# Optimization experiments

Measured on AMD Instinct MI355X. Metric: run time of the kernel, lower is better.

## Reference

```python
import jax, jax.numpy as jnp
import numpy as np

B, T, D, E, F = 4, 2048, 1024, 8, 1024

def setup_inputs() -> dict:
    key = jax.random.key(0)
    ks = jax.random.split(key, 5)
    s = lambda d: 1.0 / np.sqrt(d)
    return {
        "x": jax.random.normal(ks[0], (B, T, D), dtype=jnp.float32),
        "router_kernel_DE": jax.random.normal(ks[1], (D, E), dtype=jnp.float32) * s(D),
        "kernel_gating_EDF": jax.random.normal(ks[2], (E, D, F), dtype=jnp.float32) * s(D),
        "kernel_up_EDF": jax.random.normal(ks[3], (E, D, F), dtype=jnp.float32) * s(D),
        "kernel_down_EFD": jax.random.normal(ks[4], (E, F, D), dtype=jnp.float32) * s(F),
        "top_k": 2,
    }

def reference(x, router_kernel_DE, kernel_gating_EDF, kernel_up_EDF, kernel_down_EFD, top_k):
    # ---- Router ----
    router_logits_BTE = jnp.einsum('BTD,DE->BTE', x, router_kernel_DE)
    probs_BTE = jax.nn.softmax(router_logits_BTE.astype(jnp.float32), axis=-1)
    weights_BTX, selected_BTX = jax.lax.top_k(probs_BTE, top_k)
    # module re-normalizes top-k weights with a second softmax (faithful)
    norm_weights_BTX = jax.nn.softmax(weights_BTX, axis=-1)
    # ---- combine weights to dense per-expert weights ----
    one_hot_BTXE = jax.nn.one_hot(selected_BTX, num_classes=E, dtype=jnp.float32)
    full_weights_BTE = jnp.sum(one_hot_BTXE * norm_weights_BTX[..., None], axis=2)
    # ---- dense all-experts MLP (apply_expert_weight_before_computation=False) ----
    gating_BTEF = jnp.einsum('BTD,EDF->BTEF', x, kernel_gating_EDF)
    up_BTEF = jnp.einsum('BTD,EDF->BTEF', x, kernel_up_EDF)
    fuse_BTEF = jax.nn.silu(gating_BTEF) * up_BTEF
    down_BTED = jnp.einsum('BTEF,EFD->BTED', fuse_BTEF, kernel_down_EFD)
    out_BTD = jnp.einsum('BTED,BTE->BTD', down_BTED, full_weights_BTE)
    return out_BTD
```

## Files before the change

kernel.cpp:

```cpp
#include <hip/hip_runtime.h>
#include <hip/hip_bf16.h>
#include <math.h>

#define NTOK 8192
#define D_DIM 1024
#define E_DIM 8
#define F_DIM 1024

#define CNT_STRIDE 32

typedef __attribute__((ext_vector_type(8))) short bf16x8;
typedef __attribute__((ext_vector_type(4))) float f32x4;

typedef const __attribute__((address_space(1))) unsigned int* as1_uint_ptr;
typedef __attribute__((address_space(3))) unsigned int* as3_uint_ptr;

__device__ __forceinline__ void async_load16(const void* g, void* l) {
    __builtin_amdgcn_global_load_lds((as1_uint_ptr)g, (as3_uint_ptr)l, 16, 0, 0);
}

__device__ __forceinline__ float bf2f(unsigned short b) {
    unsigned int u = ((unsigned int)b) << 16;
    return __builtin_bit_cast(float, u);
}
__device__ __forceinline__ unsigned short f2bf(float f) {
    __hip_bfloat16 h = __float2bfloat16(f);
    return __builtin_bit_cast(unsigned short, h);
}


__global__ __launch_bounds__(512) void router_cast_kernel(
    const float* __restrict__ x,
    const float* __restrict__ Wr,
    int* __restrict__ cnt,
    int* __restrict__ tok_of,
    float* __restrict__ wt2,
    unsigned short* __restrict__ xb)
{
    __shared__ int lcnt[E_DIM];
    __shared__ int lbase[E_DIM];
    __shared__ int lbuf[E_DIM][64];

    const int tid = threadIdx.x;
    const int wv = tid >> 6;
    const int lane = tid & 63;
    if (tid < E_DIM) lcnt[tid] = 0;
    __syncthreads();

    #pragma unroll
    for (int it = 0; it < 4; ++it) {
        const int t = blockIdx.x * 32 + wv * 4 + it;
        const float* xrow = x + (size_t)t * D_DIM;
        unsigned short* xbrow = xb + (size_t)t * D_DIM;

        float p[E_DIM];
        #pragma unroll
        for (int e = 0; e < E_DIM; ++e) p[e] = 0.f;

        #pragma unroll
        for (int i = 0; i < 4; ++i) {
            const int d = i * 256 + lane * 4;
            float4 v = *(const float4*)(xrow + d);
            ushort4 o;
            o.x = f2bf(v.x); o.y = f2bf(v.y); o.z = f2bf(v.z); o.w = f2bf(v.w);
            *(ushort4*)(xbrow + d) = o;
            const float* wr = Wr + (size_t)d * E_DIM;
            float xv[4] = {v.x, v.y, v.z, v.w};
            #pragma unroll
            for (int q = 0; q < 4; ++q) {
                float4 w0 = *(const float4*)(wr + q * 8);
                float4 w1 = *(const float4*)(wr + q * 8 + 4);
                p[0] += xv[q] * w0.x; p[1] += xv[q] * w0.y;
                p[2] += xv[q] * w0.z; p[3] += xv[q] * w0.w;
                p[4] += xv[q] * w1.x; p[5] += xv[q] * w1.y;
                p[6] += xv[q] * w1.z; p[7] += xv[q] * w1.w;
            }
        }

        #pragma unroll
        for (int off = 32; off > 0; off >>= 1) {
            #pragma unroll
            for (int e = 0; e < E_DIM; ++e)
                p[e] += __shfl_xor(p[e], off, 64);
        }

        if (lane == 0) {
            float m = p[0];
            #pragma unroll
            for (int e = 1; e < E_DIM; ++e) m = fmaxf(m, p[e]);
            float pr[E_DIM], sum = 0.f;
            #pragma unroll
            for (int e = 0; e < E_DIM; ++e) { pr[e] = expf(p[e] - m); sum += pr[e]; }
            float inv = 1.f / sum;
            #pragma unroll
            for (int e = 0; e < E_DIM; ++e) pr[e] *= inv;
            int e0 = 0;
            #pragma unroll
            for (int e = 1; e < E_DIM; ++e) if (pr[e] > pr[e0]) e0 = e;
            int e1 = (e0 == 0) ? 1 : 0;
            #pragma unroll
            for (int e = 0; e < E_DIM; ++e) { if (e != e0 && pr[e] > pr[e1]) e1 = e; }
            float b = expf(pr[e1] - pr[e0]);
            float w0 = 1.f / (1.f + b);
            float w1 = b / (1.f + b);
            int p0 = atomicAdd(&lcnt[e0], 1);
            lbuf[e0][p0] = t * 2 + 0;
            int p1 = atomicAdd(&lcnt[e1], 1);
            lbuf[e1][p1] = t * 2 + 1;
            wt2[t * 2 + 0] = w0;
            wt2[t * 2 + 1] = w1;
        }
    }
    __syncthreads();
    if (tid < E_DIM) lbase[tid] = atomicAdd(&cnt[tid * CNT_STRIDE], lcnt[tid]);
    __syncthreads();
    #pragma unroll
    for (int e = 0; e < E_DIM; ++e) {
        int n = lcnt[e];
        if (tid < n) tok_of[e * NTOK + lbase[e] + tid] = lbuf[e][tid];
    }
}

__global__ __launch_bounds__(256) void transpose_cast_kernel(
    const float* __restrict__ Wg, const float* __restrict__ Wu,
    const float* __restrict__ Wd,
    unsigned short* __restrict__ WgT, unsigned short* __restrict__ WuT,
    unsigned short* __restrict__ WdT)
{
    const int m = blockIdx.z;
    const float* src;
    unsigned short* dst;
    if (m < 8)       { src = Wg + (size_t)m * 1048576;        dst = WgT + (size_t)m * 1048576; }
    else if (m < 16) { src = Wu + (size_t)(m - 8) * 1048576;  dst = WuT + (size_t)(m - 8) * 1048576; }
    else             { src = Wd + (size_t)(m - 16) * 1048576; dst = WdT + (size_t)(m - 16) * 1048576; }

    const int c0 = blockIdx.x * 64;
    const int r0 = blockIdx.y * 64;
    __shared__ float tile[64][65];
    const int tid = threadIdx.x;
    const int tr = tid >> 4;
    const int tc = (tid & 15) * 4;
    #pragma unroll
    for (int p = 0; p < 4; ++p) {
        float4 v = *(const float4*)(src + (size_t)(r0 + p * 16 + tr) * 1024 + c0 + tc);
        tile[p * 16 + tr][tc + 0] = v.x;
        tile[p * 16 + tr][tc + 1] = v.y;
        tile[p * 16 + tr][tc + 2] = v.z;
        tile[p * 16 + tr][tc + 3] = v.w;
    }
    __syncthreads();
    const int orow = tid >> 3;
    const int ocol = (tid & 7) * 8;
    #pragma unroll
    for (int p = 0; p < 2; ++p) {
        int fr = p * 32 + orow;
        union { unsigned short s[8]; uint4 v; } pk;
        #pragma unroll
        for (int q = 0; q < 8; ++q) pk.s[q] = f2bf(tile[ocol + q][fr]);
        *(uint4*)&dst[(size_t)(c0 + fr) * 1024 + r0 + ocol] = pk.v;
    }
}

__global__ __launch_bounds__(256, 2) void gateup_mfma(
    const unsigned short* __restrict__ xb,
    const unsigned short* __restrict__ WgT,
    const unsigned short* __restrict__ WuT,
    const int* __restrict__ cnt,
    const int* __restrict__ tok_of,
    unsigned short* __restrict__ H)
{
    const int e = blockIdx.y;
    const int rowTile = blockIdx.x >> 3;
    const int colTile = blockIdx.x & 7;
    const int rows = cnt[e * CNT_STRIDE];
    const int rowBase = rowTile * 128;
    if (rowBase >= rows) return;
    const int n0 = colTile * 128;

    __shared__ short As[128 * 32];
    __shared__ short Bg[128 * 32];
    __shared__ short Bu[128 * 32];
    __shared__ int toks[128];

    const int tid = threadIdx.x;
    if (tid < 128) {
        int idx = rowBase + tid;
        toks[tid] = tok_of[e * NTOK + (idx < rows ? idx : rows - 1)];
    }
    __syncthreads();

    const int lane = tid & 63;
    const int w = tid >> 6;
    const int seg0 = w * 2, seg1 = w * 2 + 1;
    const int sr = lane >> 2;
    const int swz = (sr >> 1) & 3;
    const int sk = ((lane & 3) ^ swz) * 8;

    const int ar0 = seg0 * 16 + sr;
    const int ar1 = seg1 * 16 + sr;
    const unsigned short* aG0 = xb + (size_t)(toks[ar0] >> 1) * D_DIM + sk;
    const unsigned short* aG1 = xb + (size_t)(toks[ar1] >> 1) * D_DIM + sk;
    const unsigned short* WgTe = WgT + (size_t)e * F_DIM * D_DIM;
    const unsigned short* WuTe = WuT + (size_t)e * F_DIM * D_DIM;
    const unsigned short* gG0 = WgTe + (size_t)(n0 + ar0) * D_DIM + sk;
    const unsigned short* gG1 = WgTe + (size_t)(n0 + ar1) * D_DIM + sk;
    const unsigned short* uG0 = WuTe + (size_t)(n0 + ar0) * D_DIM + sk;
    const unsigned short* uG1 = WuTe + (size_t)(n0 + ar1) * D_DIM + sk;

    short* aL0 = &As[seg0 * 512];
    short* aL1 = &As[seg1 * 512];
    short* gL0 = &Bg[seg0 * 512];
    short* gL1 = &Bg[seg1 * 512];
    short* uL0 = &Bu[seg0 * 512];
    short* uL1 = &Bu[seg1 * 512];

    const int mseg = (w >> 1) * 4;
    const int nseg = (w & 1) * 4;
    const int mbase = (w >> 1) * 64;
    const int nbase = (w & 1) * 64;
    const int fr = lane & 15;
    const int rd = (4 * fr + ((lane >> 4) ^ ((fr >> 1) & 3))) * 8;

    f32x4 accg[4][4], accu[4][4];
    #pragma unroll
    for (int i = 0; i < 4; ++i)
        #pragma unroll
        for (int j = 0; j < 4; ++j) { accg[i][j] = (f32x4)(0.f); accu[i][j] = (f32x4)(0.f); }

    for (int k0 = 0; k0 < D_DIM; k0 += 32) {
        async_load16(aG0 + k0, aL0);
        async_load16(aG1 + k0, aL1);
        async_load16(gG0 + k0, gL0);
        async_load16(gG1 + k0, gL1);
        async_load16(uG0 + k0, uL0);
        async_load16(uG1 + k0, uL1);
        __syncthreads();

        bf16x8 a[4], g[4], u[4];
        #pragma unroll
        for (int i = 0; i < 4; ++i)
            a[i] = *(const bf16x8*)&As[(mseg + i) * 512 + rd];
        #pragma unroll
        for (int j = 0; j < 4; ++j) {
            g[j] = *(const bf16x8*)&Bg[(nseg + j) * 512 + rd];
            u[j] = *(const bf16x8*)&Bu[(nseg + j) * 512 + rd];
        }
        #pragma unroll
        for (int i = 0; i < 4; ++i)
            #pragma unroll
            for (int j = 0; j < 4; ++j) {
                accg[i][j] = __builtin_amdgcn_mfma_f32_16x16x32_bf16(a[i], g[j], accg[i][j], 0, 0, 0);
                accu[i][j] = __builtin_amdgcn_mfma_f32_16x16x32_bf16(a[i], u[j], accu[i][j], 0, 0, 0);
            }
        __syncthreads();
    }

    const int erow = (lane >> 4) * 4;
    #pragma unroll
    for (int i = 0; i < 4; ++i) {
        #pragma unroll
        for (int r = 0; r < 4; ++r) {
            int row = mbase + i * 16 + erow + r;
            int idx = rowBase + row;
            if (idx < rows) {
                int tok2 = toks[row];
                unsigned short* hrow = H + (size_t)tok2 * F_DIM + n0 + nbase;
                #pragma unroll
                for (int j = 0; j < 4; ++j) {
                    float gg = accg[i][j][r];
                    float uu = accu[i][j][r];
                    float h = gg / (1.f + __expf(-gg)) * uu;
                    hrow[j * 16 + fr] = f2bf(h);
                }
            }
        }
    }
}

__global__ __launch_bounds__(256, 2) void down_mfma(
    const unsigned short* __restrict__ H,
    const unsigned short* __restrict__ WdT,
    const int* __restrict__ cnt,
    const int* __restrict__ tok_of,
    unsigned short* __restrict__ Hd)
{
    const int e = blockIdx.y;
    const int rowTile = blockIdx.x >> 3;
    const int colTile = blockIdx.x & 7;
    const int rows = cnt[e * CNT_STRIDE];
    const int rowBase = rowTile * 128;
    if (rowBase >= rows) return;
    const int n0 = colTile * 128;

    __shared__ short As[128 * 32];
    __shared__ short Bs[128 * 32];
    __shared__ int toks[128];

    const int tid = threadIdx.x;
    if (tid < 128) {
        int idx = rowBase + tid;
        toks[tid] = tok_of[e * NTOK + (idx < rows ? idx : rows - 1)];
    }
    __syncthreads();

    const int lane = tid & 63;
    const int w = tid >> 6;
    const int seg0 = w * 2, seg1 = w * 2 + 1;
    const int sr = lane >> 2;
    const int swz = (sr >> 1) & 3;
    const int sk = ((lane & 3) ^ swz) * 8;

    const int ar0 = seg0 * 16 + sr;
    const int ar1 = seg1 * 16 + sr;
    const unsigned short* aG0 = H + (size_t)toks[ar0] * F_DIM + sk;
    const unsigned short* aG1 = H + (size_t)toks[ar1] * F_DIM + sk;
    const unsigned short* WdTe = WdT + (size_t)e * D_DIM * F_DIM;
    const unsigned short* bG0 = WdTe + (size_t)(n0 + ar0) * F_DIM + sk;
    const unsigned short* bG1 = WdTe + (size_t)(n0 + ar1) * F_DIM + sk;

    short* aL0 = &As[seg0 * 512];
    short* aL1 = &As[seg1 * 512];
    short* bL0 = &Bs[seg0 * 512];
    short* bL1 = &Bs[seg1 * 512];

    const int mseg = (w >> 1) * 4;
    const int nseg = (w & 1) * 4;
    const int mbase = (w >> 1) * 64;
    const int nbase = (w & 1) * 64;
    const int fr = lane & 15;
    const int rd = (4 * fr + ((lane >> 4) ^ ((fr >> 1) & 3))) * 8;

    f32x4 acc[4][4];
    #pragma unroll
    for (int i = 0; i < 4; ++i)
        #pragma unroll
        for (int j = 0; j < 4; ++j) acc[i][j] = (f32x4)(0.f);

    for (int k0 = 0; k0 < F_DIM; k0 += 32) {
        async_load16(aG0 + k0, aL0);
        async_load16(aG1 + k0, aL1);
        async_load16(bG0 + k0, bL0);
        async_load16(bG1 + k0, bL1);
        __syncthreads();

        bf16x8 a[4], b[4];
        #pragma unroll
        for (int i = 0; i < 4; ++i)
            a[i] = *(const bf16x8*)&As[(mseg + i) * 512 + rd];
        #pragma unroll
        for (int j = 0; j < 4; ++j)
            b[j] = *(const bf16x8*)&Bs[(nseg + j) * 512 + rd];
        #pragma unroll
        for (int i = 0; i < 4; ++i)
            #pragma unroll
            for (int j = 0; j < 4; ++j)
                acc[i][j] = __builtin_amdgcn_mfma_f32_16x16x32_bf16(a[i], b[j], acc[i][j], 0, 0, 0);
        __syncthreads();
    }

    const int erow = (lane >> 4) * 4;
    #pragma unroll
    for (int i = 0; i < 4; ++i) {
        #pragma unroll
        for (int r = 0; r < 4; ++r) {
            int row = mbase + i * 16 + erow + r;
            int idx = rowBase + row;
            if (idx < rows) {
                int tok2 = toks[row];
                unsigned short* orow = Hd + (size_t)tok2 * D_DIM + n0 + nbase;
                #pragma unroll
                for (int j = 0; j < 4; ++j)
                    orow[j * 16 + fr] = f2bf(acc[i][j][r]);
            }
        }
    }
}

__global__ __launch_bounds__(256) void combine_kernel(
    const unsigned short* __restrict__ Hd,
    const float* __restrict__ wt2,
    float* __restrict__ out)
{
    const int t = blockIdx.x;
    const int tid = threadIdx.x;
    const float w0 = wt2[2 * t];
    const float w1 = wt2[2 * t + 1];
    const int c = tid * 4;
    ushort4 a = *(const ushort4*)&Hd[(size_t)(2 * t) * D_DIM + c];
    ushort4 b = *(const ushort4*)&Hd[(size_t)(2 * t + 1) * D_DIM + c];
    float4 o;
    o.x = w0 * bf2f(a.x) + w1 * bf2f(b.x);
    o.y = w0 * bf2f(a.y) + w1 * bf2f(b.y);
    o.z = w0 * bf2f(a.z) + w1 * bf2f(b.z);
    o.w = w0 * bf2f(a.w) + w1 * bf2f(b.w);
    *(float4*)(out + (size_t)t * D_DIM + c) = o;
}

extern "C" void kernel_launch(void* const* d_in, const int* in_sizes, int n_in,
                              void* d_out, int out_size, void* d_ws, size_t ws_size,
                              hipStream_t stream) {
    const float* x  = (const float*)d_in[0];
    const float* Wr = (const float*)d_in[1];
    const float* Wg = (const float*)d_in[2];
    const float* Wu = (const float*)d_in[3];
    const float* Wd = (const float*)d_in[4];
    float* out = (float*)d_out;

    char* ws = (char*)d_ws;
    int*   cnt    = (int*)ws;
    int*   tok_of = (int*)(ws + 1024);
    float* wt2    = (float*)(ws + 1024 + E_DIM * NTOK * 4);
    char*  base   = ws + (1 << 20);
    unsigned short* xb  = (unsigned short*)(base);
    unsigned short* Hd  = (unsigned short*)(base);
    unsigned short* WgT = (unsigned short*)(base + (16ll << 20));
    unsigned short* WuT = (unsigned short*)(base + (32ll << 20));
    unsigned short* WdT = (unsigned short*)(base + (48ll << 20));
    unsigned short* H   = (unsigned short*)(base + (64ll << 20));

    hipMemsetAsync(cnt, 0, E_DIM * CNT_STRIDE * sizeof(int), stream);

    router_cast_kernel<<<NTOK / 32, 512, 0, stream>>>(x, Wr, cnt, tok_of, wt2, xb);
    transpose_cast_kernel<<<dim3(16, 16, 24), 256, 0, stream>>>(Wg, Wu, Wd, WgT, WuT, WdT);

    gateup_mfma<<<dim3((NTOK / 128) * (F_DIM / 128), E_DIM), 256, 0, stream>>>(
        xb, WgT, WuT, cnt, tok_of, H);
    down_mfma<<<dim3((NTOK / 128) * (D_DIM / 128), E_DIM), 256, 0, stream>>>(
        H, WdT, cnt, tok_of, Hd);
    combine_kernel<<<NTOK, 256, 0, stream>>>(Hd, wt2, out);
}
```

Measured before the change: 373.7 us.

## Double-buffer LDS tiles with async prefetch in gate-up and down GEMMs

Both grouped MoE GEMM kernels now use two LDS buffers per operand and prefetch the tile two steps ahead with global_load_lds. Explicit vmcnt/lgkmcnt waits and raw s_barrier calls replace the two __syncthreads per K step. s_setprio is raised around the MFMA block. The aim is to hide global-memory latency behind MFMA work, at the cost of doubled LDS use, which may reduce occupancy under launch_bounds(256,2).

Result: faster. 361.4 us (-3.3%).

```diff
diff --git a/kernel.cpp b/kernel.cpp
--- a/kernel.cpp
+++ b/kernel.cpp
@@ -177,9 +177,9 @@
     if (rowBase >= rows) return;
     const int n0 = colTile * 128;
 
-    __shared__ short As[128 * 32];
-    __shared__ short Bg[128 * 32];
-    __shared__ short Bu[128 * 32];
+    __shared__ short As[2][128 * 32];
+    __shared__ short Bg[2][128 * 32];
+    __shared__ short Bu[2][128 * 32];
     __shared__ int toks[128];
 
     const int tid = threadIdx.x;
@@ -207,13 +207,6 @@
     const unsigned short* uG0 = WuTe + (size_t)(n0 + ar0) * D_DIM + sk;
     const unsigned short* uG1 = WuTe + (size_t)(n0 + ar1) * D_DIM + sk;
 
-    short* aL0 = &As[seg0 * 512];
-    short* aL1 = &As[seg1 * 512];
-    short* gL0 = &Bg[seg0 * 512];
-    short* gL1 = &Bg[seg1 * 512];
-    short* uL0 = &Bu[seg0 * 512];
-    short* uL1 = &Bu[seg1 * 512];
-
     const int mseg = (w >> 1) * 4;
     const int nseg = (w & 1) * 4;
     const int mbase = (w >> 1) * 64;
@@ -227,24 +220,40 @@
         #pragma unroll
         for (int j = 0; j < 4; ++j) { accg[i][j] = (f32x4)(0.f); accu[i][j] = (f32x4)(0.f); }
 
-    for (int k0 = 0; k0 < D_DIM; k0 += 32) {
-        async_load16(aG0 + k0, aL0);
-        async_load16(aG1 + k0, aL1);
-        async_load16(gG0 + k0, gL0);
-        async_load16(gG1 + k0, gL1);
-        async_load16(uG0 + k0, uL0);
-        async_load16(uG1 + k0, uL1);
-        __syncthreads();
+    #define STAGE_GU(b, kk) do { \
+        async_load16(aG0 + (kk), &As[b][seg0 * 512]); \
+        async_load16(aG1 + (kk), &As[b][seg1 * 512]); \
+        async_load16(gG0 + (kk), &Bg[b][seg0 * 512]); \
+        async_load16(gG1 + (kk), &Bg[b][seg1 * 512]); \
+        async_load16(uG0 + (kk), &Bu[b][seg0 * 512]); \
+        async_load16(uG1 + (kk), &Bu[b][seg1 * 512]); \
+    } while (0)
+
+    const int NT = D_DIM / 32;
+    STAGE_GU(0, 0);
+    STAGE_GU(1, 32);
+
+    #pragma unroll 2
+    for (int t = 0; t < NT - 1; ++t) {
+        const int b = t & 1;
+        asm volatile("s_waitcnt vmcnt(6)" ::: "memory");
+        __builtin_amdgcn_s_barrier();
 
         bf16x8 a[4], g[4], u[4];
         #pragma unroll
         for (int i = 0; i < 4; ++i)
-            a[i] = *(const bf16x8*)&As[(mseg + i) * 512 + rd];
+            a[i] = *(const bf16x8*)&As[b][(mseg + i) * 512 + rd];
         #pragma unroll
         for (int j = 0; j < 4; ++j) {
-            g[j] = *(const bf16x8*)&Bg[(nseg + j) * 512 + rd];
-            u[j] = *(const bf16x8*)&Bu[(nseg + j) * 512 + rd];
-        }
+            g[j] = *(const bf16x8*)&Bg[b][(nseg + j) * 512 + rd];
+            u[j] = *(const bf16x8*)&Bu[b][(nseg + j) * 512 + rd];
+        }
+        asm volatile("s_waitcnt lgkmcnt(0)" ::: "memory");
+        __builtin_amdgcn_sched_barrier(0);
+        __builtin_amdgcn_s_barrier();
+        if (t < NT - 2) STAGE_GU(b, (t + 2) * 32);
+
+        __builtin_amdgcn_s_setprio(1);
         #pragma unroll
         for (int i = 0; i < 4; ++i)
             #pragma unroll
@@ -252,8 +261,31 @@
                 accg[i][j] = __builtin_amdgcn_mfma_f32_16x16x32_bf16(a[i], g[j], accg[i][j], 0, 0, 0);
                 accu[i][j] = __builtin_amdgcn_mfma_f32_16x16x32_bf16(a[i], u[j], accu[i][j], 0, 0, 0);
             }
-        __syncthreads();
-    }
+        __builtin_amdgcn_s_setprio(0);
+    }
+    {
+        asm volatile("s_waitcnt vmcnt(0)" ::: "memory");
+        __builtin_amdgcn_s_barrier();
+        bf16x8 a[4], g[4], u[4];
+        #pragma unroll
+        for (int i = 0; i < 4; ++i)
+            a[i] = *(const bf16x8*)&As[1][(mseg + i) * 512 + rd];
+        #pragma unroll
+        for (int j = 0; j < 4; ++j) {
+            g[j] = *(const bf16x8*)&Bg[1][(nseg + j) * 512 + rd];
+            u[j] = *(const bf16x8*)&Bu[1][(nseg + j) * 512 + rd];
+        }
+        __builtin_amdgcn_s_setprio(1);
+        #pragma unroll
+        for (int i = 0; i < 4; ++i)
+            #pragma unroll
+            for (int j = 0; j < 4; ++j) {
+                accg[i][j] = __builtin_amdgcn_mfma_f32_16x16x32_bf16(a[i], g[j], accg[i][j], 0, 0, 0);
+                accu[i][j] = __builtin_amdgcn_mfma_f32_16x16x32_bf16(a[i], u[j], accu[i][j], 0, 0, 0);
+            }
+        __builtin_amdgcn_s_setprio(0);
+    }
+    #undef STAGE_GU
 
     const int erow = (lane >> 4) * 4;
     #pragma unroll
@@ -292,8 +324,8 @@
     if (rowBase >= rows) return;
     const int n0 = colTile * 128;
 
-    __shared__ short As[128 * 32];
-    __shared__ short Bs[128 * 32];
+    __shared__ short As[2][128 * 32];
+    __shared__ short Bs[2][128 * 32];
     __shared__ int toks[128];
 
     const int tid = threadIdx.x;
@@ -318,11 +350,6 @@
     const unsigned short* bG0 = WdTe + (size_t)(n0 + ar0) * F_DIM + sk;
     const unsigned short* bG1 = WdTe + (size_t)(n0 + ar1) * F_DIM + sk;
 
-    short* aL0 = &As[seg0 * 512];
-    short* aL1 = &As[seg1 * 512];
-    short* bL0 = &Bs[seg0 * 512];
-    short* bL1 = &Bs[seg1 * 512];
-
     const int mseg = (w >> 1) * 4;
     const int nseg = (w & 1) * 4;
     const int mbase = (w >> 1) * 64;
@@ -336,27 +363,63 @@
         #pragma unroll
         for (int j = 0; j < 4; ++j) acc[i][j] = (f32x4)(0.f);
 
-    for (int k0 = 0; k0 < F_DIM; k0 += 32) {
-        async_load16(aG0 + k0, aL0);
-        async_load16(aG1 + k0, aL1);
-        async_load16(bG0 + k0, bL0);
-        async_load16(bG1 + k0, bL1);
-        __syncthreads();
-
-        bf16x8 a[4], b[4];
-        #pragma unroll
-        for (int i = 0; i < 4; ++i)
-            a[i] = *(const bf16x8*)&As[(mseg + i) * 512 + rd];
+    #define STAGE_D(b, kk) do { \
+        async_load16(aG0 + (kk), &As[b][seg0 * 512]); \
+        async_load16(aG1 + (kk), &As[b][seg1 * 512]); \
+        async_load16(bG0 + (kk), &Bs[b][seg0 * 512]); \
+        async_load16(bG1 + (kk), &Bs[b][seg1 * 512]); \
+    } while (0)
+
+    const int NT = F_DIM / 32;
+    STAGE_D(0, 0);
+    STAGE_D(1, 32);
+
+    #pragma unroll 2
+    for (int t = 0; t < NT - 1; ++t) {
+        const int b = t & 1;
+        asm volatile("s_waitcnt vmcnt(4)" ::: "memory");
+        __builtin_amdgcn_s_barrier();
+
+        bf16x8 a[4], bb[4];
+        #pragma unroll
+        for (int i = 0; i < 4; ++i)
+            a[i] = *(const bf16x8*)&As[b][(mseg + i) * 512 + rd];
         #pragma unroll
         for (int j = 0; j < 4; ++j)
-            b[j] = *(const bf16x8*)&Bs[(nseg + j) * 512 + rd];
+            bb[j] = *(const bf16x8*)&Bs[b][(nseg + j) * 512 + rd];
+
+        asm volatile("s_waitcnt lgkmcnt(0)" ::: "memory");
+        __builtin_amdgcn_sched_barrier(0);
+        __builtin_amdgcn_s_barrier();
+        if (t < NT - 2) STAGE_D(b, (t + 2) * 32);
+
+        __builtin_amdgcn_s_setprio(1);
         #pragma unroll
         for (int i = 0; i < 4; ++i)
             #pragma unroll
             for (int j = 0; j < 4; ++j)
-                acc[i][j] = __builtin_amdgcn_mfma_f32_16x16x32_bf16(a[i], b[j], acc[i][j], 0, 0, 0);
-        __syncthreads();
-    }
+                acc[i][j] = __builtin_amdgcn_mfma_f32_16x16x32_bf16(a[i], bb[j], acc[i][j], 0, 0, 0);
+        __builtin_amdgcn_s_setprio(0);
+    }
+    {
+        asm volatile("s_waitcnt vmcnt(0)" ::: "memory");
+        __builtin_amdgcn_s_barrier();
+        bf16x8 a[4], bb[4];
+        #pragma unroll
+        for (int i = 0; i < 4; ++i)
+            a[i] = *(const bf16x8*)&As[1][(mseg + i) * 512 + rd];
+        #pragma unroll
+        for (int j = 0; j < 4; ++j)
+            bb[j] = *(const bf16x8*)&Bs[1][(nseg + j) * 512 + rd];
+        __builtin_amdgcn_s_setprio(1);
+        #pragma unroll
+        for (int i = 0; i < 4; ++i)
+            #pragma unroll
+            for (int j = 0; j < 4; ++j)
+                acc[i][j] = __builtin_amdgcn_mfma_f32_16x16x32_bf16(a[i], bb[j], acc[i][j], 0, 0, 0);
+        __builtin_amdgcn_s_setprio(0);
+    }
+    #undef STAGE_D
 
     const int erow = (lane >> 4) * 4;
     #pragma unroll
```

## Enlarge expert GEMM tiles and add four-stage async LDS pipeline with split phases

Applied to the files above, without the earlier changes.

Both expert GEMM kernels move to 512-thread blocks with 256-row tiles (and 256-column tiles in the down projection). Global-to-LDS loads now go through a four-buffer ring that prefetches two to three K-steps ahead, instead of a single buffer synchronized twice per step. Each K-step is split into two MFMA phases with explicit waitcnt, scheduling barriers and s_setprio, so memory latency overlaps with matrix math. This costs more LDS and accumulator registers per block, which can lower occupancy and adds tail waste on the uneven per-expert row counts.

New measurement: 378.5 us. About the same (+1.3%).

```diff
diff --git a/kernel.cpp b/kernel.cpp
--- a/kernel.cpp
+++ b/kernel.cpp
@@ -28,6 +28,10 @@
     return __builtin_bit_cast(unsigned short, h);
 }
 
+
+#define BARX() do { __builtin_amdgcn_sched_barrier(0); \
+    __builtin_amdgcn_s_barrier(); \
+    __builtin_amdgcn_sched_barrier(0); } while (0)
 
 __global__ __launch_bounds__(512) void router_cast_kernel(
     const float* __restrict__ x,
@@ -161,7 +165,7 @@
     }
 }
 
-__global__ __launch_bounds__(256, 2) void gateup_mfma(
+__global__ __launch_bounds__(512, 2) void gateup_mfma(
     const unsigned short* __restrict__ xb,
     const unsigned short* __restrict__ WgT,
     const unsigned short* __restrict__ WuT,
@@ -173,17 +177,17 @@
     const int rowTile = blockIdx.x >> 3;
     const int colTile = blockIdx.x & 7;
     const int rows = cnt[e * CNT_STRIDE];
-    const int rowBase = rowTile * 128;
+    const int rowBase = rowTile * 256;
     if (rowBase >= rows) return;
     const int n0 = colTile * 128;
 
-    __shared__ short As[128 * 32];
-    __shared__ short Bg[128 * 32];
-    __shared__ short Bu[128 * 32];
-    __shared__ int toks[128];
+    __shared__ short As[4][16 * 512];
+    __shared__ short Bg[4][8 * 512];
+    __shared__ short Bu[4][8 * 512];
+    __shared__ int toks[256];
 
     const int tid = threadIdx.x;
-    if (tid < 128) {
+    if (tid < 256) {
         int idx = rowBase + tid;
         toks[tid] = tok_of[e * NTOK + (idx < rows ? idx : rows - 1)];
     }
@@ -191,82 +195,107 @@
 
     const int lane = tid & 63;
     const int w = tid >> 6;
-    const int seg0 = w * 2, seg1 = w * 2 + 1;
     const int sr = lane >> 2;
     const int swz = (sr >> 1) & 3;
     const int sk = ((lane & 3) ^ swz) * 8;
 
-    const int ar0 = seg0 * 16 + sr;
-    const int ar1 = seg1 * 16 + sr;
-    const unsigned short* aG0 = xb + (size_t)(toks[ar0] >> 1) * D_DIM + sk;
-    const unsigned short* aG1 = xb + (size_t)(toks[ar1] >> 1) * D_DIM + sk;
+    const unsigned short* aG0 = xb + (size_t)(toks[(2 * w) * 16 + sr] >> 1) * D_DIM + sk;
+    const unsigned short* aG1 = xb + (size_t)(toks[(2 * w + 1) * 16 + sr] >> 1) * D_DIM + sk;
     const unsigned short* WgTe = WgT + (size_t)e * F_DIM * D_DIM;
     const unsigned short* WuTe = WuT + (size_t)e * F_DIM * D_DIM;
-    const unsigned short* gG0 = WgTe + (size_t)(n0 + ar0) * D_DIM + sk;
-    const unsigned short* gG1 = WgTe + (size_t)(n0 + ar1) * D_DIM + sk;
-    const unsigned short* uG0 = WuTe + (size_t)(n0 + ar0) * D_DIM + sk;
-    const unsigned short* uG1 = WuTe + (size_t)(n0 + ar1) * D_DIM + sk;
-
-    short* aL0 = &As[seg0 * 512];
-    short* aL1 = &As[seg1 * 512];
-    short* gL0 = &Bg[seg0 * 512];
-    short* gL1 = &Bg[seg1 * 512];
-    short* uL0 = &Bu[seg0 * 512];
-    short* uL1 = &Bu[seg1 * 512];
-
-    const int mseg = (w >> 1) * 4;
-    const int nseg = (w & 1) * 4;
-    const int mbase = (w >> 1) * 64;
-    const int nbase = (w & 1) * 64;
+    const unsigned short* gS = WgTe + (size_t)(n0 + w * 16 + sr) * D_DIM + sk;
+    const unsigned short* uS = WuTe + (size_t)(n0 + w * 16 + sr) * D_DIM + sk;
+
+    const int wm = w >> 2;
+    const int wn = w & 3;
     const int fr = lane & 15;
     const int rd = (4 * fr + ((lane >> 4) ^ ((fr >> 1) & 3))) * 8;
-
-    f32x4 accg[4][4], accu[4][4];
-    #pragma unroll
-    for (int i = 0; i < 4; ++i)
-        #pragma unroll
-        for (int j = 0; j < 4; ++j) { accg[i][j] = (f32x4)(0.f); accu[i][j] = (f32x4)(0.f); }
-
-    for (int k0 = 0; k0 < D_DIM; k0 += 32) {
-        async_load16(aG0 + k0, aL0);
-        async_load16(aG1 + k0, aL1);
-        async_load16(gG0 + k0, gL0);
-        async_load16(gG1 + k0, gL1);
-        async_load16(uG0 + k0, uL0);
-        async_load16(uG1 + k0, uL1);
-        __syncthreads();
-
-        bf16x8 a[4], g[4], u[4];
-        #pragma unroll
-        for (int i = 0; i < 4; ++i)
-            a[i] = *(const bf16x8*)&As[(mseg + i) * 512 + rd];
-        #pragma unroll
-        for (int j = 0; j < 4; ++j) {
-            g[j] = *(const bf16x8*)&Bg[(nseg + j) * 512 + rd];
-            u[j] = *(const bf16x8*)&Bu[(nseg + j) * 512 + rd];
-        }
-        #pragma unroll
-        for (int i = 0; i < 4; ++i)
-            #pragma unroll
-            for (int j = 0; j < 4; ++j) {
-                accg[i][j] = __builtin_amdgcn_mfma_f32_16x16x32_bf16(a[i], g[j], accg[i][j], 0, 0, 0);
-                accu[i][j] = __builtin_amdgcn_mfma_f32_16x16x32_bf16(a[i], u[j], accu[i][j], 0, 0, 0);
-            }
-        __syncthreads();
-    }
+    const int maseg = wm * 8;
+    const int nbseg = wn * 2;
+
+    f32x4 accg[8][2], accu[8][2];
+    #pragma unroll
+    for (int i = 0; i < 8; ++i)
+        #pragma unroll
+        for (int j = 0; j < 2; ++j) { accg[i][j] = (f32x4)(0.f); accu[i][j] = (f32x4)(0.f); }
+
+    bf16x8 af[4], gf[2], uf[2];
+
+    #define GU_STAGE_A(bb, kk) do { \
+        async_load16(aG0 + (kk), &As[bb][(2 * w) * 512]); \
+        async_load16(aG1 + (kk), &As[bb][(2 * w + 1) * 512]); \
+    } while (0)
+    #define GU_STAGE_B(bb, kk) do { \
+        async_load16(gS + (kk), &Bg[bb][w * 512]); \
+        async_load16(uS + (kk), &Bu[bb][w * 512]); \
+    } while (0)
+
+    #define GU_PH0(T, DOS) do { \
+        const int bb = (T) & 3; \
+        _Pragma("unroll") for (int i = 0; i < 4; ++i) \
+            af[i] = *(const bf16x8*)&As[bb][(maseg + i) * 512 + rd]; \
+        _Pragma("unroll") for (int j = 0; j < 2; ++j) { \
+            gf[j] = *(const bf16x8*)&Bg[bb][(nbseg + j) * 512 + rd]; \
+            uf[j] = *(const bf16x8*)&Bu[bb][(nbseg + j) * 512 + rd]; } \
+        if (DOS) GU_STAGE_B(((T) + 2) & 3, ((T) + 2) * 32); \
+        BARX(); \
+        __builtin_amdgcn_s_setprio(1); \
+        _Pragma("unroll") for (int i = 0; i < 4; ++i) \
+            _Pragma("unroll") for (int j = 0; j < 2; ++j) { \
+                accg[i][j] = __builtin_amdgcn_mfma_f32_16x16x32_bf16(af[i], gf[j], accg[i][j], 0, 0, 0); \
+                accu[i][j] = __builtin_amdgcn_mfma_f32_16x16x32_bf16(af[i], uf[j], accu[i][j], 0, 0, 0); } \
+        __builtin_amdgcn_s_setprio(0); \
+        BARX(); \
+    } while (0)
+
+    #define GU_PH1(T, DOS, VM) do { \
+        const int bb = (T) & 3; \
+        _Pragma("unroll") for (int i = 0; i < 4; ++i) \
+            af[i] = *(const bf16x8*)&As[bb][(maseg + 4 + i) * 512 + rd]; \
+        if (DOS) GU_STAGE_A(((T) + 3) & 3, ((T) + 3) * 32); \
+        asm volatile("s_waitcnt vmcnt(" VM ")" ::: "memory"); \
+        BARX(); \
+        __builtin_amdgcn_s_setprio(1); \
+        _Pragma("unroll") for (int i = 0; i < 4; ++i) \
+            _Pragma("unroll") for (int j = 0; j < 2; ++j) { \
+                accg[4 + i][j] = __builtin_amdgcn_mfma_f32_16x16x32_bf16(af[i], gf[j], accg[4 + i][j], 0, 0, 0); \
+                accu[4 + i][j] = __builtin_amdgcn_mfma_f32_16x16x32_bf16(af[i], uf[j], accu[4 + i][j], 0, 0, 0); } \
+        __builtin_amdgcn_s_setprio(0); \
+        BARX(); \
+    } while (0)
+
+    const int NT = D_DIM / 32;
+    GU_STAGE_A(0, 0); GU_STAGE_B(0, 0);
+    GU_STAGE_A(1, 32); GU_STAGE_B(1, 32);
+    GU_STAGE_A(2, 64);
+    asm volatile("s_waitcnt vmcnt(6)" ::: "memory");
+    BARX();
+
+    for (int t = 0; t < NT - 3; ++t) {
+        GU_PH0(t, true);
+        GU_PH1(t, true, "6");
+    }
+    GU_PH0(NT - 3, true);  GU_PH1(NT - 3, false, "4");
+    GU_PH0(NT - 2, false); GU_PH1(NT - 2, false, "0");
+    GU_PH0(NT - 1, false); GU_PH1(NT - 1, false, "0");
+
+    #undef GU_PH0
+    #undef GU_PH1
+    #undef GU_STAGE_A
+    #undef GU_STAGE_B
 
     const int erow = (lane >> 4) * 4;
     #pragma unroll
-    for (int i = 0; i < 4; ++i) {
+    for (int i = 0; i < 8; ++i) {
         #pragma unroll
         for (int r = 0; r < 4; ++r) {
-            int row = mbase + i * 16 + erow + r;
+            int row = wm * 128 + i * 16 + erow + r;
             int idx = rowBase + row;
             if (idx < rows) {
                 int tok2 = toks[row];
-                unsigned short* hrow = H + (size_t)tok2 * F_DIM + n0 + nbase;
+                unsigned short* hrow = H + (size_t)tok2 * F_DIM + n0 + wn * 32;
                 #pragma unroll
-                for (int j = 0; j < 4; ++j) {
+                for (int j = 0; j < 2; ++j) {
                     float gg = accg[i][j][r];
                     float uu = accu[i][j][r];
                     float h = gg / (1.f + __expf(-gg)) * uu;
@@ -277,7 +306,7 @@
     }
 }
 
-__global__ __launch_bounds__(256, 2) void down_mfma(
+__global__ __launch_bounds__(512, 2) void down_mfma(
     const unsigned short* __restrict__ H,
     const unsigned short* __restrict__ WdT,
     const int* __restrict__ cnt,
@@ -285,19 +314,19 @@
     unsigned short* __restrict__ Hd)
 {
     const int e = blockIdx.y;
-    const int rowTile = blockIdx.x >> 3;
-    const int colTile = blockIdx.x & 7;
+    const int rowTile = blockIdx.x >> 2;
+    const int colTile = blockIdx.x & 3;
     const int rows = cnt[e * CNT_STRIDE];
-    const int rowBase = rowTile * 128;
+    const int rowBase = rowTile * 256;
     if (rowBase >= rows) return;
-    const int n0 = colTile * 128;
-
-    __shared__ short As[128 * 32];
-    __shared__ short Bs[128 * 32];
-    __shared__ int toks[128];
+    const int n0 = colTile * 256;
+
+    __shared__ short As[4][16 * 512];
+    __shared__ short Bs[4][16 * 512];
+    __shared__ int toks[256];
 
     const int tid = threadIdx.x;
-    if (tid < 128) {
+    if (tid < 256) {
         int idx = rowBase + tid;
         toks[tid] = tok_of[e * NTOK + (idx < rows ? idx : rows - 1)];
     }
@@ -305,69 +334,101 @@
 
     const int lane = tid & 63;
     const int w = tid >> 6;
-    const int seg0 = w * 2, seg1 = w * 2 + 1;
     const int sr = lane >> 2;
     const int swz = (sr >> 1) & 3;
     const int sk = ((lane & 3) ^ swz) * 8;
 
-    const int ar0 = seg0 * 16 + sr;
-    const int ar1 = seg1 * 16 + sr;
-    const unsigned short* aG0 = H + (size_t)toks[ar0] * F_DIM + sk;
-    const unsigned short* aG1 = H + (size_t)toks[ar1] * F_DIM + sk;
+    const unsigned short* aG0 = H + (size_t)toks[(2 * w) * 16 + sr] * F_DIM + sk;
+    const unsigned short* aG1 = H + (size_t)toks[(2 * w + 1) * 16 + sr] * F_DIM + sk;
     const unsigned short* WdTe = WdT + (size_t)e * D_DIM * F_DIM;
-    const unsigned short* bG0 = WdTe + (size_t)(n0 + ar0) * F_DIM + sk;
-    const unsigned short* bG1 = WdTe + (size_t)(n0 + ar1) * F_DIM + sk;
-
-    short* aL0 = &As[seg0 * 512];
-    short* aL1 = &As[seg1 * 512];
-    short* bL0 = &Bs[seg0 * 512];
-    short* bL1 = &Bs[seg1 * 512];
-
-    const int mseg = (w >> 1) * 4;
-    const int nseg = (w & 1) * 4;
-    const int mbase = (w >> 1) * 64;
-    const int nbase = (w & 1) * 64;
+    const unsigned short* bS0 = WdTe + (size_t)(n0 + (2 * w) * 16 + sr) * F_DIM + sk;
+    const unsigned short* bS1 = WdTe + (size_t)(n0 + (2 * w + 1) * 16 + sr) * F_DIM + sk;
+
+    const int wm = w >> 2;
+    const int wn = w & 3;
     const int fr = lane & 15;
     const int rd = (4 * fr + ((lane >> 4) ^ ((fr >> 1) & 3))) * 8;
-
-    f32x4 acc[4][4];
-    #pragma unroll
-    for (int i = 0; i < 4; ++i)
+    const int maseg = wm * 8;
+    const int nbseg = wn * 4;
+
+    f32x4 acc[8][4];
+    #pragma unroll
+    for (int i = 0; i < 8; ++i)
         #pragma unroll
         for (int j = 0; j < 4; ++j) acc[i][j] = (f32x4)(0.f);
 
-    for (int k0 = 0; k0 < F_DIM; k0 += 32) {
-        async_load16(aG0 + k0, aL0);
-        async_load16(aG1 + k0, aL1);
-        async_load16(bG0 + k0, bL0);
-        async_load16(bG1 + k0, bL1);
-        __syncthreads();
-
-        bf16x8 a[4], b[4];
-        #pragma unroll
-        for (int i = 0; i < 4; ++i)
-            a[i] = *(const bf16x8*)&As[(mseg + i) * 512 + rd];
-        #pragma unroll
-        for (int j = 0; j < 4; ++j)
-            b[j] = *(const bf16x8*)&Bs[(nseg + j) * 512 + rd];
-        #pragma unroll
-        for (int i = 0; i < 4; ++i)
-            #pragma unroll
-            for (int j = 0; j < 4; ++j)
-                acc[i][j] = __builtin_amdgcn_mfma_f32_16x16x32_bf16(a[i], b[j], acc[i][j], 0, 0, 0);
-        __syncthreads();
-    }
+    bf16x8 af[4], bf[4];
+
+    #define DN_STAGE_A(bb, kk) do { \
+        async_load16(aG0 + (kk), &As[bb][(2 * w) * 512]); \
+        async_load16(aG1 + (kk), &As[bb][(2 * w + 1) * 512]); \
+    } while (0)
+    #define DN_STAGE_B(bb, kk) do { \
+        async_load16(bS0 + (kk), &Bs[bb][(2 * w) * 512]); \
+        async_load16(bS1 + (kk), &Bs[bb][(2 * w + 1) * 512]); \
+    } while (0)
+
+    #define DN_PH0(T, DOS) do { \
+        const int bb = (T) & 3; \
+        _Pragma("unroll") for (int i = 0; i < 4; ++i) \
+            af[i] = *(const bf16x8*)&As[bb][(maseg + i) * 512 + rd]; \
+        _Pragma("unroll") for (int j = 0; j < 4; ++j) \
+            bf[j] = *(const bf16x8*)&Bs[bb][(nbseg + j) * 512 + rd]; \
+        if (DOS) DN_STAGE_B(((T) + 2) & 3, ((T) + 2) * 32); \
+        BARX(); \
+        __builtin_amdgcn_s_setprio(1); \
+        _Pragma("unroll") for (int i = 0; i < 4; ++i) \
+            _Pragma("unroll") for (int j = 0; j < 4; ++j) \
+                acc[i][j] = __builtin_amdgcn_mfma_f32_16x16x32_bf16(af[i], bf[j], acc[i][j], 0, 0, 0); \
+        __builtin_amdgcn_s_setprio(0); \
+        BARX(); \
+    } while (0)
+
+    #define DN_PH1(T, DOS, VM) do { \
+        const int bb = (T) & 3; \
+        _Pragma("unroll") for (int i = 0; i < 4; ++i) \
+            af[i] = *(const bf16x8*)&As[bb][(maseg + 4 + i) * 512 + rd]; \
+        if (DOS) DN_STAGE_A(((T) + 3) & 3, ((T) + 3) * 32); \
+        asm volatile("s_waitcnt vmcnt(" VM ")" ::: "memory"); \
+        BARX(); \
+        __builtin_amdgcn_s_setprio(1); \
+        _Pragma("unroll") for (int i = 0; i < 4; ++i) \
+            _Pragma("unroll") for (int j = 0; j < 4; ++j) \
+                acc[4 + i][j] = __builtin_amdgcn_mfma_f32_16x16x32_bf16(af[i], bf[j], acc[4 + i][j], 0, 0, 0); \
+        __builtin_amdgcn_s_setprio(0); \
+        BARX(); \
+    } while (0)
+
+    const int NT = F_DIM / 32;
+    DN_STAGE_A(0, 0); DN_STAGE_B(0, 0);
+    DN_STAGE_A(1, 32); DN_STAGE_B(1, 32);
+    DN_STAGE_A(2, 64);
+    asm volatile("s_waitcnt vmcnt(6)" ::: "memory");
+    BARX();
+
+    for (int t = 0; t < NT - 3; ++t) {
+        DN_PH0(t, true);
+        DN_PH1(t, true, "6");
+    }
+    DN_PH0(NT - 3, true);  DN_PH1(NT - 3, false, "4");
+    DN_PH0(NT - 2, false); DN_PH1(NT - 2, false, "0");
+    DN_PH0(NT - 1, false); DN_PH1(NT - 1, false, "0");
+
+    #undef DN_PH0
+    #undef DN_PH1
+    #undef DN_STAGE_A
+    #undef DN_STAGE_B
 
     const int erow = (lane >> 4) * 4;
     #pragma unroll
-    for (int i = 0; i < 4; ++i) {
+    for (int i = 0; i < 8; ++i) {
         #pragma unroll
         for (int r = 0; r < 4; ++r) {
-            int row = mbase + i * 16 + erow + r;
+            int row = wm * 128 + i * 16 + erow + r;
             int idx = rowBase + row;
             if (idx < rows) {
                 int tok2 = toks[row];
-                unsigned short* orow = Hd + (size_t)tok2 * D_DIM + n0 + nbase;
+                unsigned short* orow = Hd + (size_t)tok2 * D_DIM + n0 + wn * 64;
                 #pragma unroll
                 for (int j = 0; j < 4; ++j)
                     orow[j * 16 + fr] = f2bf(acc[i][j][r]);
@@ -423,9 +484,9 @@
     router_cast_kernel<<<NTOK / 32, 512, 0, stream>>>(x, Wr, cnt, tok_of, wt2, xb);
     transpose_cast_kernel<<<dim3(16, 16, 24), 256, 0, stream>>>(Wg, Wu, Wd, WgT, WuT, WdT);
 
-    gateup_mfma<<<dim3((NTOK / 128) * (F_DIM / 128), E_DIM), 256, 0, stream>>>(
+    gateup_mfma<<<dim3(32 * 8, E_DIM), 512, 0, stream>>>(
         xb, WgT, WuT, cnt, tok_of, H);
-    down_mfma<<<dim3((NTOK / 128) * (D_DIM / 128), E_DIM), 256, 0, stream>>>(
+    down_mfma<<<dim3(32 * 4, E_DIM), 512, 0, stream>>>(
         H, WdT, cnt, tok_of, Hd);
     combine_kernel<<<NTOK, 256, 0, stream>>>(Hd, wt2, out);
 }
```
